# Kernel optimization log

Measured on AMD Instinct MI355X. Metric: run time of the kernel, lower is better.

The kernel has to match this reference:

```python
import jax, jax.numpy as jnp
from jax import lax
import numpy as np

B, N = 16, 4096
NPOINT, RADIUS, NSAMPLE = 1024, 0.2, 32
IN_CH = 64
MLP = [64, 64, 128]
EPS = 1e-5  # torch BatchNorm2d default


def setup_inputs() -> dict:
    key = jax.random.key(0)
    ks = jax.random.split(key, 2 + 2 * len(MLP))
    inp = {
        "xyz": jax.random.uniform(ks[0], (B, 3, N), jnp.float32),
        "points": jax.random.normal(ks[1], (B, IN_CH, N), jnp.float32),
    }
    last = IN_CH + 3
    for i, out in enumerate(MLP):
        inp[f"W{i}"] = jax.random.normal(ks[2 + 2 * i], (last, out), jnp.float32) / np.float32(np.sqrt(last))
        inp[f"b{i}"] = jnp.zeros((out,), jnp.float32)
        inp[f"g{i}"] = jnp.ones((out,), jnp.float32)
        inp[f"be{i}"] = jnp.zeros((out,), jnp.float32)
        last = out
    return inp


def _fps(x):
    """Farthest point sampling. x: [B,N,3] -> [B,NPOINT] int32 (start idx 0)."""
    Bv, Nn, _ = x.shape

    def step(carry, _):
        dist, far = carry
        c = jnp.take_along_axis(x, far[:, None, None], axis=1)  # [B,1,3]
        d = jnp.sum((x - c) ** 2, axis=-1)                      # [B,N]
        dist = jnp.minimum(dist, d)
        return (dist, jnp.argmax(dist, axis=-1).astype(jnp.int32)), far

    init = (jnp.full((Bv, Nn), 1e10, x.dtype), jnp.zeros((Bv,), jnp.int32))
    _, cent = lax.scan(step, init, None, length=NPOINT)
    return cent.T  # [B, NPOINT]


def _ball_query(x, new_xyz):
    """x: [B,N,3], new_xyz: [B,S,3] -> idx [B,S,NSAMPLE] int32."""
    Nn = x.shape[1]
    sqr = jnp.sum((new_xyz[:, :, None, :] - x[:, None, :, :]) ** 2, axis=-1)  # [B,S,N]
    idx = jnp.where(sqr > RADIUS ** 2, Nn, jnp.arange(Nn, dtype=jnp.int32))
    idx = jnp.sort(idx, axis=-1)[:, :, :NSAMPLE]  # first NSAMPLE in-radius indices
    first = idx[:, :, :1]
    return jnp.where(idx == Nn, first, idx)


def _gather(pts, idx):
    """pts: [B,N,C], idx: [B,S,K] -> [B,S,K,C]."""
    Bv, S, K = idx.shape
    flat = idx.reshape(Bv, S * K)
    return jnp.take_along_axis(pts, flat[:, :, None], axis=1).reshape(Bv, S, K, pts.shape[-1])


def _forward(xyz, points, params):
    x = xyz.transpose(0, 2, 1)      # [B,N,3]
    p = points.transpose(0, 2, 1)   # [B,N,D]
    fps_idx = _fps(x)
    new_xyz = jnp.take_along_axis(x, fps_idx[:, :, None], axis=1)  # [B,S,3]
    idx = _ball_query(x, new_xyz)
    g_xyz = _gather(x, idx) - new_xyz[:, :, None, :]               # [B,S,K,3]
    feats = jnp.concatenate([g_xyz, _gather(p, idx)], axis=-1)     # [B,S,K,3+D]
    for (W, b, g, be) in params:
        feats = jnp.einsum('bskc,cd->bskd', feats, W) + b          # 1x1 conv
        mean = feats.mean(axis=(0, 1, 2))                          # BN train-mode batch stats
        var = feats.var(axis=(0, 1, 2))
        feats = jax.nn.relu(g * (feats - mean) * lax.rsqrt(var + EPS) + be)
    new_points = feats.max(axis=2).transpose(0, 2, 1)              # max over nsample -> [B,C',S]
    return new_xyz.transpose(0, 2, 1), new_points


def reference(xyz, points, W0, b0, g0, be0, W1, b1, g1, be1, W2, b2, g2, be2):
    params = [(W0, b0, g0, be0), (W1, b1, g1, be1), (W2, b2, g2, be2)]
    return _forward(xyz, points, params)
```

## Files before the change

kernel.cpp:

```cpp
#include <hip/hip_runtime.h>
#include <hip/hip_bf16.h>
#include <cstdint>


typedef __attribute__((ext_vector_type(8))) short bf16x8;
typedef __attribute__((ext_vector_type(4))) float f32x4;

#define LDA 104

__device__ __forceinline__ unsigned short f2bf(float f) {
  unsigned x = __float_as_uint(f);
  unsigned r = (x + 0x7FFFu + ((x >> 16) & 1u)) >> 16;
  return (unsigned short)r;
}
__device__ __forceinline__ float bf2f(unsigned short u) {
  return __uint_as_float(((unsigned)u) << 16);
}

template <int CTRL>
__device__ __forceinline__ unsigned long long dppmax(unsigned long long k) {
  int lo = (int)(unsigned)k;
  int hi = (int)(unsigned)(k >> 32);
  int plo = __builtin_amdgcn_update_dpp(lo, lo, CTRL, 0xF, 0xF, false);
  int phi = __builtin_amdgcn_update_dpp(hi, hi, CTRL, 0xF, 0xF, false);
  unsigned long long o =
      ((unsigned long long)(unsigned)phi << 32) | (unsigned)plo;
  return (o > k) ? o : k;
}

__device__ __forceinline__ void spin_ge(int* p, int need) {
  while (__hip_atomic_load(p, __ATOMIC_ACQUIRE, __HIP_MEMORY_SCOPE_AGENT) < need)
    __builtin_amdgcn_s_sleep(32);
}

__global__ __attribute__((amdgpu_flat_work_group_size(256, 256),
                          amdgpu_waves_per_eu(1, 1)))
void mega_kernel(
    const float* __restrict__ xyz, const float* __restrict__ points,
    const float* __restrict__ W0, const float* __restrict__ W1,
    const float* __restrict__ W2, const float* __restrict__ b0,
    unsigned short* __restrict__ pT, unsigned short* __restrict__ w0t,
    unsigned short* __restrict__ w1t, unsigned short* __restrict__ w2t,
    float4* __restrict__ centers4, unsigned short* __restrict__ feats1,
    float* __restrict__ partials, float* __restrict__ out,
    int* __restrict__ ctrl)
{
  __shared__ __align__(16) char smraw[61568];
  __shared__ int tkt_s;
  int tid = threadIdx.x;
  int bx = blockIdx.x;
  int* progress  = ctrl;
  int* prep_done = ctrl + 16;
  int* g1_ticket = ctrl + 17;

  if (bx < 16) {
    float* xs  = (float*)smraw;
    float* ys  = xs + 4096;
    float* zs  = ys + 4096;
    float* cxl = zs + 4096;
    float* cyl = cxl + 1024;
    float* czl = cyl + 1024;
    unsigned long long (*keybuf)[4] =
        (unsigned long long (*)[4])(smraw + 61440);

    int b = bx;
    const float* xb = xyz + (size_t)b * 12288;
    float px[16], py[16], pz[16], dist[16];
#pragma unroll
    for (int j = 0; j < 16; ++j) {
      int n = tid + (j << 8);
      px[j] = xb[n]; py[j] = xb[4096 + n]; pz[j] = xb[8192 + n];
      xs[n] = px[j]; ys[n] = py[j]; zs[n] = pz[j];
      dist[j] = 1e10f;
    }
    __syncthreads();
    float cx = xs[0], cy = ys[0], cz = zs[0];
    if (tid == 0) { cxl[0] = cx; cyl[0] = cy; czl[0] = cz; }
    int w = tid >> 6;
    int lane = tid & 63;
    int it = 1;
#pragma unroll 1
    for (int seg = 0; seg < 16; ++seg) {
      int itend = (seg + 1) << 6;
#pragma unroll 1
      for (; it < itend; ++it) {
        float bv = -1.f; int bi = 0;
#pragma unroll
        for (int j = 0; j < 16; ++j) {
          float dx = __fsub_rn(px[j], cx);
          float dy = __fsub_rn(py[j], cy);
          float dz = __fsub_rn(pz[j], cz);
          float d  = __fadd_rn(__fadd_rn(__fmul_rn(dx, dx), __fmul_rn(dy, dy)),
                               __fmul_rn(dz, dz));
          float nd = fminf(dist[j], d);
          dist[j] = nd;
          if (nd > bv) { bv = nd; bi = tid + (j << 8); }
        }
        unsigned long long k =
            ((unsigned long long)__float_as_uint(bv) << 32) | (unsigned)(~bi);
        k = dppmax<0xB1>(k);
        k = dppmax<0x4E>(k);
        k = dppmax<0x141>(k);
        k = dppmax<0x140>(k);
        k = dppmax<0x142>(k);
        k = dppmax<0x143>(k);
        int p = it & 1;
        if (lane == 63) keybuf[p][w] = k;
        __syncthreads();
        uint4 ka2 = *(const uint4*)&keybuf[p][0];
        uint4 kb2 = *(const uint4*)&keybuf[p][2];
        unsigned long long k0 = ((unsigned long long)ka2.y << 32) | ka2.x;
        unsigned long long k1 = ((unsigned long long)ka2.w << 32) | ka2.z;
        unsigned long long k2 = ((unsigned long long)kb2.y << 32) | kb2.x;
        unsigned long long k3 = ((unsigned long long)kb2.w << 32) | kb2.z;
        unsigned long long m01 = (k1 > k0) ? k1 : k0;
        unsigned long long m23 = (k3 > k2) ? k3 : k2;
        unsigned long long km  = (m23 > m01) ? m23 : m01;
        int gi = (int)(~(unsigned)km) & 4095;
        cx = xs[gi]; cy = ys[gi]; cz = zs[gi];
        if (tid == 0) { cxl[it] = cx; cyl[it] = cy; czl[it] = cz; }
      }
      if (seg < 15) {
        if (tid < 64) {
          int s = (seg << 6) + tid;
          centers4[(b << 10) + s] = make_float4(cxl[s], cyl[s], czl[s], 0.f);
        }
        if (tid == 0) {
          __threadfence();
          __hip_atomic_store(&progress[b], itend, __ATOMIC_RELEASE,
                             __HIP_MEMORY_SCOPE_AGENT);
        }
      }
    }
    __syncthreads();
    for (int s = tid; s < 1024; s += 256) {
      float x = cxl[s], y = cyl[s], z = czl[s];
      out[b * 3072 + s]        = x;
      out[b * 3072 + 1024 + s] = y;
      out[b * 3072 + 2048 + s] = z;
      centers4[(b << 10) + s]  = make_float4(x, y, z, 0.f);
    }
    __syncthreads();
    if (tid == 0) {
      __threadfence();
      __hip_atomic_store(&progress[b], 1024, __ATOMIC_RELEASE,
                         __HIP_MEMORY_SCOPE_AGENT);
    }
  } else {
    int wid = bx - 16;
    int cnt = 0;
    for (int t = wid; t < 1025; t += 240) {
      __syncthreads();
      if (t < 1024) {
        float (*tile)[65] = (float (*)[65])smraw;
        int b = t >> 6;
        int n0 = (t & 63) << 6;
        const float* pbp = points + ((size_t)b << 18);
        for (int i = tid; i < 4096; i += 256) {
          int cc = i >> 6, nn = i & 63;
          tile[cc][nn] = pbp[((size_t)cc << 12) + n0 + nn];
        }
        __syncthreads();
        for (int i = tid; i < 4096; i += 256) {
          int nn = i >> 6, cc = i & 63;
          pT[(((size_t)((b << 12) + n0 + nn)) << 6) + cc] = f2bf(tile[cc][nn]);
        }
      } else {
        for (int i = tid; i < 26624; i += 256) {
          if (i < 6656) {
            int nn = i / 104, kk = i % 104;
            float v = (kk < 64) ? W0[(3 + kk) * 64 + nn]
                                : ((kk < 67) ? W0[(kk - 64) * 64 + nn] : 0.f);
            w0t[i] = f2bf(v);
          } else if (i < 13312) {
            int j = i - 6656; int nn = j / 104, kk = j % 104;
            w1t[j] = f2bf((kk < 64) ? W1[kk * 64 + nn] : 0.f);
          } else {
            int j = i - 13312; int nn = j / 104, kk = j % 104;
            w2t[j] = f2bf((kk < 64) ? W2[kk * 128 + nn] : 0.f);
          }
        }
      }
      ++cnt;
    }
    __syncthreads();
    if (tid == 0) {
      __threadfence();
      __hip_atomic_fetch_add(prep_done, cnt, __ATOMIC_RELEASE,
                             __HIP_MEMORY_SCOPE_AGENT);
    }
  }

  spin_ge(prep_done, 1025);
  __syncthreads();

  float* xs = (float*)smraw;
  float* ys = xs + 4096;
  float* zs = ys + 4096;
  unsigned short* As = (unsigned short*)smraw;
  unsigned short* Wt = (unsigned short*)(smraw + 13312);
  float* red = (float*)(smraw + 26624);
  int* idxl = (int*)(smraw + 60416);

  int lane = tid & 63, w = tid >> 6;
  int mrow = (w << 4) + (lane & 15);
  int quad = lane >> 4;
  unsigned long long lmask = (1ull << lane) - 1ull;

  for (;;) {
    if (tid == 0) tkt_s = atomicAdd(g1_ticket, 1);
    __syncthreads();
    int tk = tkt_s;
    if (tk >= 2048) break;
    int tile = ((tk & 15) << 7) | (tk >> 4);
    int b = tile >> 7;
    int s0 = (tile & 127) << 3;
    spin_ge(&progress[b], s0 + 8);

    {
      const float* xb = xyz + (size_t)b * 12288;
      for (int i = tid; i < 4096; i += 256) {
        xs[i] = xb[i]; ys[i] = xb[4096 + i]; zs[i] = xb[8192 + i];
      }
    }
    __syncthreads();
    {
      int cg0 = (b << 10) + s0;
      for (int c2 = 0; c2 < 2; ++c2) {
        int sl = (w << 1) + c2;
        float4 c = centers4[cg0 + sl];
        int* ob = idxl + (sl << 5);
        int cnt2 = 0, first = 0;
        for (int m = 0; m < 64; ++m) {
          int n = (m << 6) + lane;
          float dx = __fsub_rn(xs[n], c.x);
          float dy = __fsub_rn(ys[n], c.y);
          float dz = __fsub_rn(zs[n], c.z);
          float d  = __fadd_rn(__fadd_rn(__fmul_rn(dx, dx), __fmul_rn(dy, dy)),
                               __fmul_rn(dz, dz));
          bool hit = !(d > 0.04f);
          unsigned long long mask = __ballot(hit);
          if (cnt2 == 0 && mask != 0ull)
            first = (m << 6) + (__ffsll((long long)mask) - 1);
          int p = cnt2 + (int)__popcll(mask & lmask);
          if (hit && p < 32) ob[p] = n;
          cnt2 += (int)__popcll(mask);
          if (cnt2 >= 32) break;
        }
        if (lane < 32 && lane >= cnt2) ob[lane] = first;
      }
    }
    __syncthreads();

    {
      const uint4* wsrc = (const uint4*)w0t;
      uint4* wdst = (uint4*)Wt;
      for (int i = tid; i < 832; i += 256) wdst[i] = wsrc[i];
    }
    float a0acc = 0.f, a1acc = 0.f;
    for (int tt = 0; tt < 4; ++tt) {
      int rowbase = (tile << 8) + (tt << 6);
      {
        int rl = tid >> 2, part = tid & 3;
        int n = idxl[(tt << 6) + rl];
        const uint4* psrc = (const uint4*)(pT + (((size_t)((b << 12) + n)) << 6));
        uint4* adst = (uint4*)(As + rl * LDA);
        adst[part * 2]     = psrc[part * 2];
        adst[part * 2 + 1] = psrc[part * 2 + 1];
        adst[8 + part] = make_uint4(0, 0, 0, 0);
        if (part == 0) {
          int r = rowbase + rl;
          float4 c = centers4[r >> 5];
          unsigned short* arow = As + rl * LDA;
          arow[64] = f2bf(__fsub_rn(xyz[(size_t)b * 12288 + n],        c.x));
          arow[65] = f2bf(__fsub_rn(xyz[(size_t)b * 12288 + 4096 + n], c.y));
          arow[66] = f2bf(__fsub_rn(xyz[(size_t)b * 12288 + 8192 + n], c.z));
        }
      }
      __syncthreads();
      f32x4 acc[4];
#pragma unroll
      for (int nt = 0; nt < 4; ++nt) acc[nt] = (f32x4){0.f, 0.f, 0.f, 0.f};
#pragma unroll
      for (int kt = 0; kt < 3; ++kt) {
        int ko = kt * 32 + (quad << 3);
        bf16x8 a = *(const bf16x8*)(As + mrow * LDA + ko);
#pragma unroll
        for (int nt = 0; nt < 4; ++nt) {
          bf16x8 bb = *(const bf16x8*)(Wt + ((nt << 4) + (lane & 15)) * LDA + ko);
          acc[nt] = __builtin_amdgcn_mfma_f32_16x16x32_bf16(a, bb, acc[nt], 0, 0, 0);
        }
      }
#pragma unroll
      for (int nt = 0; nt < 4; ++nt) {
        int cch = (nt << 4) + (lane & 15);
        float bias = b0[cch];
        float ssum = 0.f, sq = 0.f;
#pragma unroll
        for (int r2 = 0; r2 < 4; ++r2) {
          float y = acc[nt][r2] + bias;
          int ml = (w << 4) + (quad << 2) + r2;
          feats1[(((size_t)(rowbase + ml)) << 6) + cch] = f2bf(y);
          ssum += y; sq += y * y;
        }
        ssum += __shfl_xor(ssum, 16); ssum += __shfl_xor(ssum, 32);
        sq   += __shfl_xor(sq, 16);   sq   += __shfl_xor(sq, 32);
        if (quad == 0) { red[w * 64 + cch] = ssum; red[256 + w * 64 + cch] = sq; }
      }
      __syncthreads();
      if (tid < 64) {
        a0acc += red[tid] + red[64 + tid] + red[128 + tid] + red[192 + tid];
        a1acc += red[256 + tid] + red[320 + tid] + red[384 + tid] + red[448 + tid];
      }
    }
    if (tid < 64) {
      partials[(size_t)tile * 256 + tid]      = a0acc;
      partials[(size_t)tile * 256 + 64 + tid] = a1acc;
    }
    __syncthreads();
  }
}

__global__ __launch_bounds__(256) void gemm2_kernel(
    const unsigned short* __restrict__ featsIn, const unsigned short* __restrict__ wt,
    const float* __restrict__ bias_g, const float* __restrict__ ss_in,
    unsigned short* __restrict__ featsOut, float* __restrict__ partials)
{
  __shared__ unsigned short As[64 * LDA];
  __shared__ unsigned short Wt[64 * LDA];
  __shared__ float red[2][4][64];
  __shared__ float ssl[128];
  int tid = threadIdx.x;
  int blockbase = blockIdx.x << 8;
  if (tid < 128) ssl[tid] = ss_in[tid];
  {
    const uint4* wsrc = (const uint4*)wt;
    uint4* wdst = (uint4*)Wt;
    for (int i = tid; i < 832; i += 256) wdst[i] = wsrc[i];
  }
  int lane = tid & 63, w = tid >> 6;
  int mrow = (w << 4) + (lane & 15);
  int quad = lane >> 4;
  float a0acc = 0.f, a1acc = 0.f;
  __syncthreads();
  for (int t = 0; t < 4; ++t) {
    int rowbase = blockbase + (t << 6);
    {
      int rl = tid >> 2, part = tid & 3;
      size_t r = (size_t)rowbase + rl;
      union { uint4 v[2]; unsigned short u[16]; } tt;
      const uint4* src = (const uint4*)(featsIn + (r << 6));
      tt.v[0] = src[part * 2]; tt.v[1] = src[part * 2 + 1];
      union { uint4 v[2]; unsigned short u[16]; } o;
#pragma unroll
      for (int e = 0; e < 16; ++e) {
        int cch = (part << 4) + e;
        float f = bf2f(tt.u[e]);
        float y = fmaxf(f * ssl[cch] + ssl[64 + cch], 0.f);
        o.u[e] = f2bf(y);
      }
      uint4* adst = (uint4*)(As + rl * LDA + (part << 4));
      adst[0] = o.v[0]; adst[1] = o.v[1];
    }
    __syncthreads();
    f32x4 acc[4];
#pragma unroll
    for (int nt = 0; nt < 4; ++nt) acc[nt] = (f32x4){0.f, 0.f, 0.f, 0.f};
#pragma unroll
    for (int kt = 0; kt < 2; ++kt) {
      int ko = kt * 32 + (quad << 3);
      bf16x8 a = *(const bf16x8*)(As + mrow * LDA + ko);
#pragma unroll
      for (int nt = 0; nt < 4; ++nt) {
        bf16x8 bb = *(const bf16x8*)(Wt + ((nt << 4) + (lane & 15)) * LDA + ko);
        acc[nt] = __builtin_amdgcn_mfma_f32_16x16x32_bf16(a, bb, acc[nt], 0, 0, 0);
      }
    }
#pragma unroll
    for (int nt = 0; nt < 4; ++nt) {
      int cch = (nt << 4) + (lane & 15);
      float bias = bias_g[cch];
      float ssum = 0.f, sq = 0.f;
#pragma unroll
      for (int r2 = 0; r2 < 4; ++r2) {
        float y = acc[nt][r2] + bias;
        int ml = (w << 4) + (quad << 2) + r2;
        featsOut[(((size_t)(rowbase + ml)) << 6) + cch] = f2bf(y);
        ssum += y; sq += y * y;
      }
      ssum += __shfl_xor(ssum, 16); ssum += __shfl_xor(ssum, 32);
      sq   += __shfl_xor(sq, 16);   sq   += __shfl_xor(sq, 32);
      if (quad == 0) { red[0][w][cch] = ssum; red[1][w][cch] = sq; }
    }
    __syncthreads();
    if (tid < 64) {
      a0acc += red[0][0][tid] + red[0][1][tid] + red[0][2][tid] + red[0][3][tid];
      a1acc += red[1][0][tid] + red[1][1][tid] + red[1][2][tid] + red[1][3][tid];
    }
  }
  if (tid < 64) {
    partials[(size_t)blockIdx.x * 256 + tid]      = a0acc;
    partials[(size_t)blockIdx.x * 256 + 64 + tid] = a1acc;
  }
}

__global__ __launch_bounds__(256) void gemm3_stats_kernel(
    const unsigned short* __restrict__ feats2, const unsigned short* __restrict__ w2t,
    const float* __restrict__ b2, const float* __restrict__ ss2,
    float* __restrict__ partials, float* __restrict__ y3mx,
    float* __restrict__ y3mn)
{
  __shared__ unsigned short As[64 * LDA];
  __shared__ unsigned short Wt[128 * LDA];
  __shared__ float red[2][4][128];
  __shared__ float mxw[4][128];
  __shared__ float mnw[4][128];
  __shared__ float ssl[128];
  int tid = threadIdx.x;
  int blockbase = blockIdx.x << 8;
  if (tid < 128) ssl[tid] = ss2[tid];
  {
    const uint4* wsrc = (const uint4*)w2t;
    uint4* wdst = (uint4*)Wt;
    for (int i = tid; i < 1664; i += 256) wdst[i] = wsrc[i];
  }
  int lane = tid & 63, w = tid >> 6;
  int mrow = (w << 4) + (lane & 15);
  int quad = lane >> 4;
  float a0acc = 0.f, a1acc = 0.f;
  __syncthreads();
  for (int t = 0; t < 4; ++t) {
    int rowbase = blockbase + (t << 6);
    {
      int rl = tid >> 2, part = tid & 3;
      size_t r = (size_t)rowbase + rl;
      union { uint4 v[2]; unsigned short u[16]; } tt;
      const uint4* src = (const uint4*)(feats2 + (r << 6));
      tt.v[0] = src[part * 2]; tt.v[1] = src[part * 2 + 1];
      union { uint4 v[2]; unsigned short u[16]; } o;
#pragma unroll
      for (int e = 0; e < 16; ++e) {
        int cch = (part << 4) + e;
        float f = bf2f(tt.u[e]);
        float y = fmaxf(f * ssl[cch] + ssl[64 + cch], 0.f);
        o.u[e] = f2bf(y);
      }
      uint4* adst = (uint4*)(As + rl * LDA + (part << 4));
      adst[0] = o.v[0]; adst[1] = o.v[1];
    }
    __syncthreads();
    f32x4 acc[8];
#pragma unroll
    for (int nt = 0; nt < 8; ++nt) acc[nt] = (f32x4){0.f, 0.f, 0.f, 0.f};
#pragma unroll
    for (int kt = 0; kt < 2; ++kt) {
      int ko = kt * 32 + (quad << 3);
      bf16x8 a = *(const bf16x8*)(As + mrow * LDA + ko);
#pragma unroll
      for (int nt = 0; nt < 8; ++nt) {
        bf16x8 bb = *(const bf16x8*)(Wt + ((nt << 4) + (lane & 15)) * LDA + ko);
        acc[nt] = __builtin_amdgcn_mfma_f32_16x16x32_bf16(a, bb, acc[nt], 0, 0, 0);
      }
    }
#pragma unroll
    for (int nt = 0; nt < 8; ++nt) {
      int cch = (nt << 4) + (lane & 15);
      float bias = b2[cch];
      float ssum = 0.f, sq = 0.f;
      float mx = -3.4e38f, mn = 3.4e38f;
#pragma unroll
      for (int r2 = 0; r2 < 4; ++r2) {
        float y = acc[nt][r2] + bias;
        ssum += y; sq += y * y;
        mx = fmaxf(mx, y); mn = fminf(mn, y);
      }
      ssum += __shfl_xor(ssum, 16); ssum += __shfl_xor(ssum, 32);
      sq   += __shfl_xor(sq, 16);   sq   += __shfl_xor(sq, 32);
      mx = fmaxf(mx, __shfl_xor(mx, 16)); mx = fmaxf(mx, __shfl_xor(mx, 32));
      mn = fminf(mn, __shfl_xor(mn, 16)); mn = fminf(mn, __shfl_xor(mn, 32));
      if (quad == 0) {
        red[0][w][cch] = ssum; red[1][w][cch] = sq;
        mxw[w][cch] = mx; mnw[w][cch] = mn;
      }
    }
    __syncthreads();
    if (tid < 128) {
      a0acc += red[0][0][tid] + red[0][1][tid] + red[0][2][tid] + red[0][3][tid];
      a1acc += red[1][0][tid] + red[1][1][tid] + red[1][2][tid] + red[1][3][tid];
    }
    {
      int c2 = tid >> 7, cch = tid & 127;
      int cg = (rowbase >> 5) + c2;
      y3mx[((size_t)cg << 7) + cch] = fmaxf(mxw[2 * c2][cch], mxw[2 * c2 + 1][cch]);
      y3mn[((size_t)cg << 7) + cch] = fminf(mnw[2 * c2][cch], mnw[2 * c2 + 1][cch]);
    }
  }
  if (tid < 128) {
    partials[(size_t)blockIdx.x * 256 + tid]       = a0acc;
    partials[(size_t)blockIdx.x * 256 + 128 + tid] = a1acc;
  }
}

__global__ __launch_bounds__(256) void reduce_kernel(const float* __restrict__ partials,
                                                     float* __restrict__ stats, int twoC)
{
  int tid = threadIdx.x;
  if (tid < twoC) {
    int row0 = blockIdx.x << 5;
    float s = 0.f;
    for (int r = 0; r < 32; ++r) s += partials[((size_t)(row0 + r)) * 256 + tid];
    atomicAdd(&stats[tid], s);
  }
}

__global__ void finalize_kernel(const float* __restrict__ stats, const float* __restrict__ g,
                                const float* __restrict__ be, float* __restrict__ ss, int C)
{
  int c = threadIdx.x;
  if (c < C) {
    const float invM = 1.f / 524288.f;
    float mean = stats[c] * invM;
    float ex2  = stats[C + c] * invM;
    float var  = ex2 - mean * mean;
    float sc   = g[c] / sqrtf(var + 1e-5f);
    ss[c]     = sc;
    ss[C + c] = be[c] - mean * sc;
  }
}

__global__ __launch_bounds__(256) void bn3_out_kernel(
    const float* __restrict__ y3mx, const float* __restrict__ y3mn,
    const float* __restrict__ ss3, float* __restrict__ out)
{
  __shared__ float t2[64][65];
  __shared__ float sl[128];
  int tid = threadIdx.x;
  int b = blockIdx.x >> 5;
  int rest = blockIdx.x & 31;
  int s0 = (rest & 15) << 6;
  int c0 = (rest >> 4) << 6;
  if (tid < 64) sl[tid] = ss3[c0 + tid];
  else if (tid < 128) sl[tid] = ss3[128 + c0 + (tid - 64)];
  __syncthreads();
  for (int i = tid; i < 4096; i += 256) {
    int row = i >> 6, col = i & 63;
    size_t cg = (size_t)((b << 10) + s0 + row);
    float mx = y3mx[(cg << 7) + c0 + col];
    float mn = y3mn[(cg << 7) + c0 + col];
    float sc = sl[col], sh = sl[64 + col];
    float ye = (sc >= 0.f) ? mx : mn;
    t2[row][col] = fmaxf(ye * sc + sh, 0.f);
  }
  __syncthreads();
  for (int i = tid; i < 4096; i += 256) {
    int crow = i >> 6, scol = i & 63;
    out[49152 + ((size_t)b << 17) + (size_t)(c0 + crow) * 1024 + s0 + scol] = t2[scol][crow];
  }
}

extern "C" void kernel_launch(void* const* d_in, const int* in_sizes, int n_in,
                              void* d_out, int out_size, void* d_ws, size_t ws_size,
                              hipStream_t stream)
{
  (void)in_sizes; (void)n_in; (void)out_size; (void)ws_size;
  const float* xyz    = (const float*)d_in[0];
  const float* points = (const float*)d_in[1];
  const float* W0  = (const float*)d_in[2];
  const float* b0  = (const float*)d_in[3];
  const float* g0  = (const float*)d_in[4];
  const float* be0 = (const float*)d_in[5];
  const float* W1  = (const float*)d_in[6];
  const float* b1  = (const float*)d_in[7];
  const float* g1  = (const float*)d_in[8];
  const float* be1 = (const float*)d_in[9];
  const float* W2  = (const float*)d_in[10];
  const float* b2  = (const float*)d_in[11];
  const float* g2  = (const float*)d_in[12];
  const float* be2 = (const float*)d_in[13];
  float* out = (float*)d_out;

  char* base = (char*)d_ws;
  size_t off = 0;
  auto alloc = [&](size_t bytes) -> void* {
    void* p = base + off;
    off += (bytes + 255) & ~(size_t)255;
    return p;
  };
  unsigned short* pT     = (unsigned short*)alloc((size_t)16 * 4096 * 64 * 2);
  unsigned short* w0t    = (unsigned short*)alloc(64 * LDA * 2);
  unsigned short* w1t    = (unsigned short*)alloc(64 * LDA * 2);
  unsigned short* w2t    = (unsigned short*)alloc(128 * LDA * 2);
  float* stats_all       = (float*)alloc(512 * 4);
  float* ss_all          = (float*)alloc(512 * 4);
  float4* centers4       = (float4*)alloc((size_t)16 * 1024 * 16);
  unsigned short* feats1 = (unsigned short*)alloc((size_t)524288 * 64 * 2);
  unsigned short* feats2 = (unsigned short*)alloc((size_t)524288 * 64 * 2);
  float* partials        = (float*)alloc((size_t)2048 * 256 * 4);
  int* ctrl              = (int*)alloc(4096);

  float* y3mx = (float*)feats1;
  float* y3mn = y3mx + (size_t)16384 * 128;

  float* stats1 = stats_all;       float* stats2 = stats_all + 128; float* stats3 = stats_all + 256;
  float* ss1 = ss_all;             float* ss2 = ss_all + 128;       float* ss3 = ss_all + 256;

  hipMemsetAsync(ctrl, 0, 4096, stream);
  hipMemsetAsync(stats_all, 0, 512 * 4, stream);

  void* kargs[15] = {
    (void*)&xyz, (void*)&points, (void*)&W0, (void*)&W1, (void*)&W2,
    (void*)&b0, (void*)&pT, (void*)&w0t, (void*)&w1t, (void*)&w2t,
    (void*)&centers4, (void*)&feats1, (void*)&partials, (void*)&out,
    (void*)&ctrl
  };
  if (hipLaunchCooperativeKernel((void*)mega_kernel, dim3(256), dim3(256),
                                 kargs, 0, stream) != hipSuccess) {
    mega_kernel<<<256, 256, 0, stream>>>(xyz, points, W0, W1, W2, b0, pT, w0t,
                                         w1t, w2t, centers4, feats1, partials,
                                         out, ctrl);
  }
  reduce_kernel<<<64, 256, 0, stream>>>(partials, stats1, 128);
  finalize_kernel<<<1, 64, 0, stream>>>(stats1, g0, be0, ss1, 64);
  gemm2_kernel<<<2048, 256, 0, stream>>>(feats1, w1t, b1, ss1, feats2, partials);
  reduce_kernel<<<64, 256, 0, stream>>>(partials, stats2, 128);
  finalize_kernel<<<1, 64, 0, stream>>>(stats2, g1, be1, ss2, 64);
  gemm3_stats_kernel<<<2048, 256, 0, stream>>>(feats2, w2t, b2, ss2, partials, y3mx, y3mn);
  reduce_kernel<<<64, 256, 0, stream>>>(partials, stats3, 256);
  finalize_kernel<<<1, 128, 0, stream>>>(stats3, g2, be2, ss3, 128);
  bn3_out_kernel<<<512, 256, 0, stream>>>(y3mx, y3mn, ss3, out);
}
```

Measured before the change: 893.9 us.

## Fold BN stat reduce/finalize into consumer kernels via atomic grid junction

Removes the separate reduce and finalize kernel launches between the GEMM stages. Instead, the first 64 blocks of each consumer kernel reduce the previous stage's partials, and the last one to finish computes the scale/shift and raises a ready flag that every block spins on. The change also drops redundant __threadfence calls before release atomics and makes the feats1 stores nontemporal. The cost is spin-waiting blocks that occupy CUs while the reducers run, and a reliance on in-order block dispatch so the grid cannot deadlock.

```diff
diff --git a/kernel.cpp b/kernel.cpp
--- a/kernel.cpp
+++ b/kernel.cpp
@@ -126,7 +126,6 @@
           centers4[(b << 10) + s] = make_float4(cxl[s], cyl[s], czl[s], 0.f);
         }
         if (tid == 0) {
-          __threadfence();
           __hip_atomic_store(&progress[b], itend, __ATOMIC_RELEASE,
                              __HIP_MEMORY_SCOPE_AGENT);
         }
@@ -142,7 +141,6 @@
     }
     __syncthreads();
     if (tid == 0) {
-      __threadfence();
       __hip_atomic_store(&progress[b], 1024, __ATOMIC_RELEASE,
                          __HIP_MEMORY_SCOPE_AGENT);
     }
@@ -185,7 +183,6 @@
     }
     __syncthreads();
     if (tid == 0) {
-      __threadfence();
       __hip_atomic_fetch_add(prep_done, cnt, __ATOMIC_RELEASE,
                              __HIP_MEMORY_SCOPE_AGENT);
     }
@@ -300,7 +297,8 @@
         for (int r2 = 0; r2 < 4; ++r2) {
           float y = acc[nt][r2] + bias;
           int ml = (w << 4) + (quad << 2) + r2;
-          feats1[(((size_t)(rowbase + ml)) << 6) + cch] = f2bf(y);
+          __builtin_nontemporal_store(
+              f2bf(y), feats1 + (((size_t)(rowbase + ml)) << 6) + cch);
           ssum += y; sq += y * y;
         }
         ssum += __shfl_xor(ssum, 16); ssum += __shfl_xor(ssum, 32);
@@ -321,23 +319,66 @@
   }
 }
 
+__device__ __forceinline__ void stats_junction(
+    int bxx, int tid, const float* __restrict__ partials_prev, float* stats,
+    const float* __restrict__ g, const float* __restrict__ be, float* ss,
+    int* rcnt, int* rdy, int twoC, int C, int* lastf )
+{
+  if (bxx < 64) {
+    if (tid < twoC) {
+      int row0 = bxx << 5;
+      float s = 0.f;
+      for (int r = 0; r < 32; ++r)
+        s += partials_prev[((size_t)(row0 + r)) * 256 + tid];
+      atomicAdd(&stats[tid], s);
+    }
+    __syncthreads();
+    if (tid == 0) {
+      int prev = __hip_atomic_fetch_add(rcnt, 1, __ATOMIC_ACQ_REL,
+                                        __HIP_MEMORY_SCOPE_AGENT);
+      *lastf = (prev == 63) ? 1 : 0;
+    }
+    __syncthreads();
+    if (*lastf) {
+      if (tid < C) {
+        const float invM = 1.f / 524288.f;
+        float mean = stats[tid] * invM;
+        float ex2  = stats[C + tid] * invM;
+        float var  = ex2 - mean * mean;
+        float sc   = g[tid] / sqrtf(var + 1e-5f);
+        ss[tid]     = sc;
+        ss[C + tid] = be[tid] - mean * sc;
+      }
+      __syncthreads();
+      if (tid == 0)
+        __hip_atomic_store(rdy, 1, __ATOMIC_RELEASE, __HIP_MEMORY_SCOPE_AGENT);
+    }
+  }
+  spin_ge(rdy, 1);
+}
+
 __global__ __launch_bounds__(256) void gemm2_kernel(
     const unsigned short* __restrict__ featsIn, const unsigned short* __restrict__ wt,
-    const float* __restrict__ bias_g, const float* __restrict__ ss_in,
-    unsigned short* __restrict__ featsOut, float* __restrict__ partials)
+    const float* __restrict__ bias_g, float* partials,
+    float* stats, const float* __restrict__ g, const float* __restrict__ be,
+    float* ss, int* rcnt, int* rdy,
+    unsigned short* __restrict__ featsOut)
 {
   __shared__ unsigned short As[64 * LDA];
   __shared__ unsigned short Wt[64 * LDA];
   __shared__ float red[2][4][64];
   __shared__ float ssl[128];
+  __shared__ int lastf;
   int tid = threadIdx.x;
   int blockbase = blockIdx.x << 8;
-  if (tid < 128) ssl[tid] = ss_in[tid];
   {
     const uint4* wsrc = (const uint4*)wt;
     uint4* wdst = (uint4*)Wt;
     for (int i = tid; i < 832; i += 256) wdst[i] = wsrc[i];
   }
+  stats_junction(blockIdx.x, tid, partials, stats, g, be, ss, rcnt, rdy,
+                 128, 64, &lastf);
+  if (tid < 128) ssl[tid] = ss[tid];
   int lane = tid & 63, w = tid >> 6;
   int mrow = (w << 4) + (lane & 15);
   int quad = lane >> 4;
@@ -406,9 +447,10 @@
 
 __global__ __launch_bounds__(256) void gemm3_stats_kernel(
     const unsigned short* __restrict__ feats2, const unsigned short* __restrict__ w2t,
-    const float* __restrict__ b2, const float* __restrict__ ss2,
-    float* __restrict__ partials, float* __restrict__ y3mx,
-    float* __restrict__ y3mn)
+    const float* __restrict__ b2, float* partials,
+    float* stats, const float* __restrict__ g, const float* __restrict__ be,
+    float* ss, int* rcnt, int* rdy,
+    float* __restrict__ y3mx, float* __restrict__ y3mn)
 {
   __shared__ unsigned short As[64 * LDA];
   __shared__ unsigned short Wt[128 * LDA];
@@ -416,14 +458,17 @@
   __shared__ float mxw[4][128];
   __shared__ float mnw[4][128];
   __shared__ float ssl[128];
+  __shared__ int lastf;
   int tid = threadIdx.x;
   int blockbase = blockIdx.x << 8;
-  if (tid < 128) ssl[tid] = ss2[tid];
   {
     const uint4* wsrc = (const uint4*)w2t;
     uint4* wdst = (uint4*)Wt;
     for (int i = tid; i < 1664; i += 256) wdst[i] = wsrc[i];
   }
+  stats_junction(blockIdx.x, tid, partials, stats, g, be, ss, rcnt, rdy,
+                 128, 64, &lastf);
+  if (tid < 128) ssl[tid] = ss[tid];
   int lane = tid & 63, w = tid >> 6;
   int mrow = (w << 4) + (lane & 15);
   int quad = lane >> 4;
@@ -501,46 +546,25 @@
   }
 }
 
-__global__ __launch_bounds__(256) void reduce_kernel(const float* __restrict__ partials,
-                                                     float* __restrict__ stats, int twoC)
-{
-  int tid = threadIdx.x;
-  if (tid < twoC) {
-    int row0 = blockIdx.x << 5;
-    float s = 0.f;
-    for (int r = 0; r < 32; ++r) s += partials[((size_t)(row0 + r)) * 256 + tid];
-    atomicAdd(&stats[tid], s);
-  }
-}
-
-__global__ void finalize_kernel(const float* __restrict__ stats, const float* __restrict__ g,
-                                const float* __restrict__ be, float* __restrict__ ss, int C)
-{
-  int c = threadIdx.x;
-  if (c < C) {
-    const float invM = 1.f / 524288.f;
-    float mean = stats[c] * invM;
-    float ex2  = stats[C + c] * invM;
-    float var  = ex2 - mean * mean;
-    float sc   = g[c] / sqrtf(var + 1e-5f);
-    ss[c]     = sc;
-    ss[C + c] = be[c] - mean * sc;
-  }
-}
-
 __global__ __launch_bounds__(256) void bn3_out_kernel(
     const float* __restrict__ y3mx, const float* __restrict__ y3mn,
-    const float* __restrict__ ss3, float* __restrict__ out)
+    const float* __restrict__ partials,
+    float* stats, const float* __restrict__ g, const float* __restrict__ be,
+    float* ss, int* rcnt, int* rdy,
+    float* __restrict__ out)
 {
   __shared__ float t2[64][65];
   __shared__ float sl[128];
+  __shared__ int lastf;
   int tid = threadIdx.x;
+  stats_junction(blockIdx.x, tid, partials, stats, g, be, ss, rcnt, rdy,
+                 256, 128, &lastf);
   int b = blockIdx.x >> 5;
   int rest = blockIdx.x & 31;
   int s0 = (rest & 15) << 6;
   int c0 = (rest >> 4) << 6;
-  if (tid < 64) sl[tid] = ss3[c0 + tid];
-  else if (tid < 128) sl[tid] = ss3[128 + c0 + (tid - 64)];
+  if (tid < 64) sl[tid] = ss[c0 + tid];
+  else if (tid < 128) sl[tid] = ss[128 + c0 + (tid - 64)];
   __syncthreads();
   for (int i = tid; i < 4096; i += 256) {
     int row = i >> 6, col = i & 63;
@@ -604,6 +628,10 @@
   float* stats1 = stats_all;       float* stats2 = stats_all + 128; float* stats3 = stats_all + 256;
   float* ss1 = ss_all;             float* ss2 = ss_all + 128;       float* ss3 = ss_all + 256;
 
+  int* rcnt1 = ctrl + 18; int* rdy1 = ctrl + 19;
+  int* rcnt2 = ctrl + 20; int* rdy2 = ctrl + 21;
+  int* rcnt3 = ctrl + 22; int* rdy3 = ctrl + 23;
+
   hipMemsetAsync(ctrl, 0, 4096, stream);
   hipMemsetAsync(stats_all, 0, 512 * 4, stream);
 
@@ -619,13 +647,11 @@
                                          w1t, w2t, centers4, feats1, partials,
                                          out, ctrl);
   }
-  reduce_kernel<<<64, 256, 0, stream>>>(partials, stats1, 128);
-  finalize_kernel<<<1, 64, 0, stream>>>(stats1, g0, be0, ss1, 64);
-  gemm2_kernel<<<2048, 256, 0, stream>>>(feats1, w1t, b1, ss1, feats2, partials);
-  reduce_kernel<<<64, 256, 0, stream>>>(partials, stats2, 128);
-  finalize_kernel<<<1, 64, 0, stream>>>(stats2, g1, be1, ss2, 64);
-  gemm3_stats_kernel<<<2048, 256, 0, stream>>>(feats2, w2t, b2, ss2, partials, y3mx, y3mn);
-  reduce_kernel<<<64, 256, 0, stream>>>(partials, stats3, 256);
-  finalize_kernel<<<1, 128, 0, stream>>>(stats3, g2, be2, ss3, 128);
-  bn3_out_kernel<<<512, 256, 0, stream>>>(y3mx, y3mn, ss3, out);
-}
+  gemm2_kernel<<<2048, 256, 0, stream>>>(feats1, w1t, b1, partials, stats1,
+                                         g0, be0, ss1, rcnt1, rdy1, feats2);
+  gemm3_stats_kernel<<<2048, 256, 0, stream>>>(feats2, w2t, b2, partials, stats2,
+                                               g1, be1, ss2, rcnt2, rdy2,
+                                               y3mx, y3mn);
+  bn3_out_kernel<<<512, 256, 0, stream>>>(y3mx, y3mn, partials, stats3,
+                                          g2, be2, ss3, rcnt3, rdy3, out);
+}
```

New measurement: 1.347 ms. 50.7% more time.

## Load MFMA A-operands directly from global and drop per-tile LDS staging and barriers

Applied to the files above, without the earlier changes.

The gemm2 and gemm3 kernels no longer stage the BN+ReLU-transformed activations through an LDS tile. Each lane now loads its MFMA A fragment straight from global memory, with scale and shift held in registers, and each wave processes its own 64 rows with no per-tile __syncthreads. Statistics and min/max are accumulated in registers and reduced across waves once at the end. Redundant __threadfence calls before the release atomics in the fused FPS/prep kernel are also removed. The aim is to cut LDS traffic and barrier stalls, at the cost of less coalesced global reads and higher register pressure.

```diff
diff --git a/kernel.cpp b/kernel.cpp
--- a/kernel.cpp
+++ b/kernel.cpp
@@ -5,6 +5,7 @@
 
 typedef __attribute__((ext_vector_type(8))) short bf16x8;
 typedef __attribute__((ext_vector_type(4))) float f32x4;
+union f4u { float4 v; float f[4]; };
 
 #define LDA 104
 
@@ -126,7 +127,6 @@
           centers4[(b << 10) + s] = make_float4(cxl[s], cyl[s], czl[s], 0.f);
         }
         if (tid == 0) {
-          __threadfence();
           __hip_atomic_store(&progress[b], itend, __ATOMIC_RELEASE,
                              __HIP_MEMORY_SCOPE_AGENT);
         }
@@ -142,7 +142,6 @@
     }
     __syncthreads();
     if (tid == 0) {
-      __threadfence();
       __hip_atomic_store(&progress[b], 1024, __ATOMIC_RELEASE,
                          __HIP_MEMORY_SCOPE_AGENT);
     }
@@ -185,7 +184,6 @@
     }
     __syncthreads();
     if (tid == 0) {
-      __threadfence();
       __hip_atomic_fetch_add(prep_done, cnt, __ATOMIC_RELEASE,
                              __HIP_MEMORY_SCOPE_AGENT);
     }
@@ -326,81 +324,87 @@
     const float* __restrict__ bias_g, const float* __restrict__ ss_in,
     unsigned short* __restrict__ featsOut, float* __restrict__ partials)
 {
-  __shared__ unsigned short As[64 * LDA];
   __shared__ unsigned short Wt[64 * LDA];
   __shared__ float red[2][4][64];
-  __shared__ float ssl[128];
   int tid = threadIdx.x;
   int blockbase = blockIdx.x << 8;
-  if (tid < 128) ssl[tid] = ss_in[tid];
   {
     const uint4* wsrc = (const uint4*)wt;
     uint4* wdst = (uint4*)Wt;
     for (int i = tid; i < 832; i += 256) wdst[i] = wsrc[i];
   }
   int lane = tid & 63, w = tid >> 6;
-  int mrow = (w << 4) + (lane & 15);
+  int col = lane & 15;
   int quad = lane >> 4;
-  float a0acc = 0.f, a1acc = 0.f;
+  int q8 = quad << 3;
+  f4u sc0a, sc0b, sh0a, sh0b, sc1a, sc1b, sh1a, sh1b;
+  sc0a.v = *(const float4*)(ss_in + q8);
+  sc0b.v = *(const float4*)(ss_in + q8 + 4);
+  sh0a.v = *(const float4*)(ss_in + 64 + q8);
+  sh0b.v = *(const float4*)(ss_in + 64 + q8 + 4);
+  sc1a.v = *(const float4*)(ss_in + 32 + q8);
+  sc1b.v = *(const float4*)(ss_in + 32 + q8 + 4);
+  sh1a.v = *(const float4*)(ss_in + 96 + q8);
+  sh1b.v = *(const float4*)(ss_in + 96 + q8 + 4);
+  float bias[4];
+#pragma unroll
+  for (int nt = 0; nt < 4; ++nt) bias[nt] = bias_g[(nt << 4) + col];
+  float wsum[4] = {0.f, 0.f, 0.f, 0.f}, wsq[4] = {0.f, 0.f, 0.f, 0.f};
   __syncthreads();
-  for (int t = 0; t < 4; ++t) {
-    int rowbase = blockbase + (t << 6);
-    {
-      int rl = tid >> 2, part = tid & 3;
-      size_t r = (size_t)rowbase + rl;
-      union { uint4 v[2]; unsigned short u[16]; } tt;
-      const uint4* src = (const uint4*)(featsIn + (r << 6));
-      tt.v[0] = src[part * 2]; tt.v[1] = src[part * 2 + 1];
-      union { uint4 v[2]; unsigned short u[16]; } o;
-#pragma unroll
-      for (int e = 0; e < 16; ++e) {
-        int cch = (part << 4) + e;
-        float f = bf2f(tt.u[e]);
-        float y = fmaxf(f * ssl[cch] + ssl[64 + cch], 0.f);
-        o.u[e] = f2bf(y);
-      }
-      uint4* adst = (uint4*)(As + rl * LDA + (part << 4));
-      adst[0] = o.v[0]; adst[1] = o.v[1];
-    }
-    __syncthreads();
+#pragma unroll
+  for (int mt = 0; mt < 4; ++mt) {
+    int rowl = (w << 6) + (mt << 4) + col;
+    const unsigned short* src = featsIn + (((size_t)(blockbase + rowl)) << 6);
+    union { bf16x8 v; unsigned short u[8]; } r0, r1, a0, a1;
+    r0.v = *(const bf16x8*)(src + q8);
+    r1.v = *(const bf16x8*)(src + 32 + q8);
+#pragma unroll
+    for (int e = 0; e < 4; ++e) {
+      a0.u[e]     = f2bf(fmaxf(bf2f(r0.u[e])     * sc0a.f[e] + sh0a.f[e], 0.f));
+      a0.u[4 + e] = f2bf(fmaxf(bf2f(r0.u[4 + e]) * sc0b.f[e] + sh0b.f[e], 0.f));
+      a1.u[e]     = f2bf(fmaxf(bf2f(r1.u[e])     * sc1a.f[e] + sh1a.f[e], 0.f));
+      a1.u[4 + e] = f2bf(fmaxf(bf2f(r1.u[4 + e]) * sc1b.f[e] + sh1b.f[e], 0.f));
+    }
     f32x4 acc[4];
 #pragma unroll
     for (int nt = 0; nt < 4; ++nt) acc[nt] = (f32x4){0.f, 0.f, 0.f, 0.f};
 #pragma unroll
-    for (int kt = 0; kt < 2; ++kt) {
-      int ko = kt * 32 + (quad << 3);
-      bf16x8 a = *(const bf16x8*)(As + mrow * LDA + ko);
-#pragma unroll
-      for (int nt = 0; nt < 4; ++nt) {
-        bf16x8 bb = *(const bf16x8*)(Wt + ((nt << 4) + (lane & 15)) * LDA + ko);
-        acc[nt] = __builtin_amdgcn_mfma_f32_16x16x32_bf16(a, bb, acc[nt], 0, 0, 0);
-      }
-    }
-#pragma unroll
     for (int nt = 0; nt < 4; ++nt) {
-      int cch = (nt << 4) + (lane & 15);
-      float bias = bias_g[cch];
+      const unsigned short* wrow = Wt + ((nt << 4) + col) * LDA;
+      bf16x8 bb0 = *(const bf16x8*)(wrow + q8);
+      bf16x8 bb1 = *(const bf16x8*)(wrow + 32 + q8);
+      acc[nt] = __builtin_amdgcn_mfma_f32_16x16x32_bf16(a0.v, bb0, acc[nt], 0, 0, 0);
+      acc[nt] = __builtin_amdgcn_mfma_f32_16x16x32_bf16(a1.v, bb1, acc[nt], 0, 0, 0);
+    }
+#pragma unroll
+    for (int nt = 0; nt < 4; ++nt) {
+      int cch = (nt << 4) + col;
       float ssum = 0.f, sq = 0.f;
 #pragma unroll
       for (int r2 = 0; r2 < 4; ++r2) {
-        float y = acc[nt][r2] + bias;
-        int ml = (w << 4) + (quad << 2) + r2;
-        featsOut[(((size_t)(rowbase + ml)) << 6) + cch] = f2bf(y);
+        float y = acc[nt][r2] + bias[nt];
+        int ml = (w << 6) + (mt << 4) + (quad << 2) + r2;
+        featsOut[(((size_t)(blockbase + ml)) << 6) + cch] = f2bf(y);
         ssum += y; sq += y * y;
       }
       ssum += __shfl_xor(ssum, 16); ssum += __shfl_xor(ssum, 32);
       sq   += __shfl_xor(sq, 16);   sq   += __shfl_xor(sq, 32);
-      if (quad == 0) { red[0][w][cch] = ssum; red[1][w][cch] = sq; }
-    }
-    __syncthreads();
-    if (tid < 64) {
-      a0acc += red[0][0][tid] + red[0][1][tid] + red[0][2][tid] + red[0][3][tid];
-      a1acc += red[1][0][tid] + red[1][1][tid] + red[1][2][tid] + red[1][3][tid];
-    }
-  }
+      wsum[nt] += ssum; wsq[nt] += sq;
+    }
+  }
+  if (quad == 0) {
+#pragma unroll
+    for (int nt = 0; nt < 4; ++nt) {
+      red[0][w][(nt << 4) + col] = wsum[nt];
+      red[1][w][(nt << 4) + col] = wsq[nt];
+    }
+  }
+  __syncthreads();
   if (tid < 64) {
-    partials[(size_t)blockIdx.x * 256 + tid]      = a0acc;
-    partials[(size_t)blockIdx.x * 256 + 64 + tid] = a1acc;
+    float a0 = red[0][0][tid] + red[0][1][tid] + red[0][2][tid] + red[0][3][tid];
+    float a1 = red[1][0][tid] + red[1][1][tid] + red[1][2][tid] + red[1][3][tid];
+    partials[(size_t)blockIdx.x * 256 + tid]      = a0;
+    partials[(size_t)blockIdx.x * 256 + 64 + tid] = a1;
   }
 }
 
@@ -410,67 +414,67 @@
     float* __restrict__ partials, float* __restrict__ y3mx,
     float* __restrict__ y3mn)
 {
-  __shared__ unsigned short As[64 * LDA];
   __shared__ unsigned short Wt[128 * LDA];
   __shared__ float red[2][4][128];
-  __shared__ float mxw[4][128];
-  __shared__ float mnw[4][128];
-  __shared__ float ssl[128];
   int tid = threadIdx.x;
   int blockbase = blockIdx.x << 8;
-  if (tid < 128) ssl[tid] = ss2[tid];
   {
     const uint4* wsrc = (const uint4*)w2t;
     uint4* wdst = (uint4*)Wt;
     for (int i = tid; i < 1664; i += 256) wdst[i] = wsrc[i];
   }
   int lane = tid & 63, w = tid >> 6;
-  int mrow = (w << 4) + (lane & 15);
+  int col = lane & 15;
   int quad = lane >> 4;
-  float a0acc = 0.f, a1acc = 0.f;
+  int q8 = quad << 3;
+  f4u sc0a, sc0b, sh0a, sh0b, sc1a, sc1b, sh1a, sh1b;
+  sc0a.v = *(const float4*)(ss2 + q8);
+  sc0b.v = *(const float4*)(ss2 + q8 + 4);
+  sh0a.v = *(const float4*)(ss2 + 64 + q8);
+  sh0b.v = *(const float4*)(ss2 + 64 + q8 + 4);
+  sc1a.v = *(const float4*)(ss2 + 32 + q8);
+  sc1b.v = *(const float4*)(ss2 + 32 + q8 + 4);
+  sh1a.v = *(const float4*)(ss2 + 96 + q8);
+  sh1b.v = *(const float4*)(ss2 + 96 + q8 + 4);
+  float bias[8];
+#pragma unroll
+  for (int nt = 0; nt < 8; ++nt) bias[nt] = b2[(nt << 4) + col];
+  float wsum[8], wsq[8], cmx[8], cmn[8];
+#pragma unroll
+  for (int nt = 0; nt < 8; ++nt) { wsum[nt] = 0.f; wsq[nt] = 0.f; }
   __syncthreads();
-  for (int t = 0; t < 4; ++t) {
-    int rowbase = blockbase + (t << 6);
-    {
-      int rl = tid >> 2, part = tid & 3;
-      size_t r = (size_t)rowbase + rl;
-      union { uint4 v[2]; unsigned short u[16]; } tt;
-      const uint4* src = (const uint4*)(feats2 + (r << 6));
-      tt.v[0] = src[part * 2]; tt.v[1] = src[part * 2 + 1];
-      union { uint4 v[2]; unsigned short u[16]; } o;
-#pragma unroll
-      for (int e = 0; e < 16; ++e) {
-        int cch = (part << 4) + e;
-        float f = bf2f(tt.u[e]);
-        float y = fmaxf(f * ssl[cch] + ssl[64 + cch], 0.f);
-        o.u[e] = f2bf(y);
-      }
-      uint4* adst = (uint4*)(As + rl * LDA + (part << 4));
-      adst[0] = o.v[0]; adst[1] = o.v[1];
-    }
-    __syncthreads();
+#pragma unroll
+  for (int mt = 0; mt < 4; ++mt) {
+    int rowl = (w << 6) + (mt << 4) + col;
+    const unsigned short* src = feats2 + (((size_t)(blockbase + rowl)) << 6);
+    union { bf16x8 v; unsigned short u[8]; } r0, r1, a0, a1;
+    r0.v = *(const bf16x8*)(src + q8);
+    r1.v = *(const bf16x8*)(src + 32 + q8);
+#pragma unroll
+    for (int e = 0; e < 4; ++e) {
+      a0.u[e]     = f2bf(fmaxf(bf2f(r0.u[e])     * sc0a.f[e] + sh0a.f[e], 0.f));
+      a0.u[4 + e] = f2bf(fmaxf(bf2f(r0.u[4 + e]) * sc0b.f[e] + sh0b.f[e], 0.f));
+      a1.u[e]     = f2bf(fmaxf(bf2f(r1.u[e])     * sc1a.f[e] + sh1a.f[e], 0.f));
+      a1.u[4 + e] = f2bf(fmaxf(bf2f(r1.u[4 + e]) * sc1b.f[e] + sh1b.f[e], 0.f));
+    }
     f32x4 acc[8];
 #pragma unroll
     for (int nt = 0; nt < 8; ++nt) acc[nt] = (f32x4){0.f, 0.f, 0.f, 0.f};
 #pragma unroll
-    for (int kt = 0; kt < 2; ++kt) {
-      int ko = kt * 32 + (quad << 3);
-      bf16x8 a = *(const bf16x8*)(As + mrow * LDA + ko);
-#pragma unroll
-      for (int nt = 0; nt < 8; ++nt) {
-        bf16x8 bb = *(const bf16x8*)(Wt + ((nt << 4) + (lane & 15)) * LDA + ko);
-        acc[nt] = __builtin_amdgcn_mfma_f32_16x16x32_bf16(a, bb, acc[nt], 0, 0, 0);
-      }
-    }
-#pragma unroll
     for (int nt = 0; nt < 8; ++nt) {
-      int cch = (nt << 4) + (lane & 15);
-      float bias = b2[cch];
+      const unsigned short* wrow = Wt + ((nt << 4) + col) * LDA;
+      bf16x8 bb0 = *(const bf16x8*)(wrow + q8);
+      bf16x8 bb1 = *(const bf16x8*)(wrow + 32 + q8);
+      acc[nt] = __builtin_amdgcn_mfma_f32_16x16x32_bf16(a0.v, bb0, acc[nt], 0, 0, 0);
+      acc[nt] = __builtin_amdgcn_mfma_f32_16x16x32_bf16(a1.v, bb1, acc[nt], 0, 0, 0);
+    }
+#pragma unroll
+    for (int nt = 0; nt < 8; ++nt) {
       float ssum = 0.f, sq = 0.f;
       float mx = -3.4e38f, mn = 3.4e38f;
 #pragma unroll
       for (int r2 = 0; r2 < 4; ++r2) {
-        float y = acc[nt][r2] + bias;
+        float y = acc[nt][r2] + bias[nt];
         ssum += y; sq += y * y;
         mx = fmaxf(mx, y); mn = fminf(mn, y);
       }
@@ -478,26 +482,35 @@
       sq   += __shfl_xor(sq, 16);   sq   += __shfl_xor(sq, 32);
       mx = fmaxf(mx, __shfl_xor(mx, 16)); mx = fmaxf(mx, __shfl_xor(mx, 32));
       mn = fminf(mn, __shfl_xor(mn, 16)); mn = fminf(mn, __shfl_xor(mn, 32));
+      wsum[nt] += ssum; wsq[nt] += sq;
+      if ((mt & 1) == 0) { cmx[nt] = mx; cmn[nt] = mn; }
+      else               { cmx[nt] = fmaxf(cmx[nt], mx); cmn[nt] = fminf(cmn[nt], mn); }
+    }
+    if (mt & 1) {
+      int cg = (blockbase >> 5) + (w << 1) + (mt >> 1);
       if (quad == 0) {
-        red[0][w][cch] = ssum; red[1][w][cch] = sq;
-        mxw[w][cch] = mx; mnw[w][cch] = mn;
-      }
-    }
-    __syncthreads();
-    if (tid < 128) {
-      a0acc += red[0][0][tid] + red[0][1][tid] + red[0][2][tid] + red[0][3][tid];
-      a1acc += red[1][0][tid] + red[1][1][tid] + red[1][2][tid] + red[1][3][tid];
-    }
-    {
-      int c2 = tid >> 7, cch = tid & 127;
-      int cg = (rowbase >> 5) + c2;
-      y3mx[((size_t)cg << 7) + cch] = fmaxf(mxw[2 * c2][cch], mxw[2 * c2 + 1][cch]);
-      y3mn[((size_t)cg << 7) + cch] = fminf(mnw[2 * c2][cch], mnw[2 * c2 + 1][cch]);
-    }
-  }
+#pragma unroll
+        for (int nt = 0; nt < 8; ++nt) {
+          int cch = (nt << 4) + col;
+          y3mx[((size_t)cg << 7) + cch] = cmx[nt];
+          y3mn[((size_t)cg << 7) + cch] = cmn[nt];
+        }
+      }
+    }
+  }
+  if (quad == 0) {
+#pragma unroll
+    for (int nt = 0; nt < 8; ++nt) {
+      red[0][w][(nt << 4) + col] = wsum[nt];
+      red[1][w][(nt << 4) + col] = wsq[nt];
+    }
+  }
+  __syncthreads();
   if (tid < 128) {
-    partials[(size_t)blockIdx.x * 256 + tid]       = a0acc;
-    partials[(size_t)blockIdx.x * 256 + 128 + tid] = a1acc;
+    float a0 = red[0][0][tid] + red[0][1][tid] + red[0][2][tid] + red[0][3][tid];
+    float a1 = red[1][0][tid] + red[1][1][tid] + red[1][2][tid] + red[1][3][tid];
+    partials[(size_t)blockIdx.x * 256 + tid]       = a0;
+    partials[(size_t)blockIdx.x * 256 + 128 + tid] = a1;
   }
 }
 
```

After: 920.6 us. 1.03x slower.
